# Optimization experiments

Hardware: AMD Instinct MI355X
Metric: run time of the kernel (lower is better)

Reference implementation:

```python
import jax, jax.numpy as jnp
import numpy as np

N, D_IN, D_OUT, E = 100000, 64, 64, 1600000


def setup_inputs() -> dict:
    key = jax.random.key(0)
    k1, k2, k3, k4, k5 = jax.random.split(key, 5)
    x = jax.random.normal(k1, (N, D_IN), dtype=jnp.float32)
    edge_index = jax.random.randint(k2, (2, E), 0, N, dtype=jnp.int64)
    # Linear params (PyTorch default: uniform(-1/sqrt(fan_in), 1/sqrt(fan_in)))
    bound = 1.0 / np.sqrt(D_IN)
    W_self = jax.random.uniform(k3, (D_IN, D_OUT), jnp.float32, -bound, bound)
    b_self = jnp.zeros((D_OUT,), jnp.float32)
    W_neigh = jax.random.uniform(k4, (D_IN, D_OUT), jnp.float32, -bound, bound)
    b_neigh = jax.random.uniform(k5, (D_OUT,), jnp.float32, -bound, bound)
    return {"x": x, "edge_index": edge_index, "W_self": W_self,
            "b_self": b_self, "W_neigh": W_neigh, "b_neigh": b_neigh}


def reference(x, edge_index, W_self, b_self, W_neigh, b_neigh):
    src, dst = edge_index[0], edge_index[1]
    # gather messages from source nodes, scatter-add into destinations
    agg = jax.ops.segment_sum(x[src], dst, num_segments=x.shape[0])  # [N, D_IN]
    # in-degree, clamped to >= 1 (matches bincount().clamp_min(1))
    deg = jax.ops.segment_sum(jnp.ones_like(dst, dtype=x.dtype), dst,
                              num_segments=x.shape[0])
    deg = jnp.maximum(deg, 1.0)[:, None]
    agg = agg / deg
    h = x @ W_self + b_self + agg @ W_neigh + b_neigh
    # dropout is identity in eval mode
    return jax.nn.relu(h)
```

## Files before the change

### kernel.cpp

```cpp
#include <hip/hip_runtime.h>


#define D 64
#define P 256
#define CVTB 1024
#define WTB 4
#define NBMAX 512
#define NP 392
#define BN 256
#define SORTCAP 8160
#define KP 136

typedef __attribute__((ext_vector_type(8))) short bf8_t;
typedef __attribute__((ext_vector_type(4))) float f4_t;

__device__ inline unsigned int bf_rn(float f) {
  unsigned int u = __float_as_uint(f);
  return (u + 0x7FFFu + ((u >> 16) & 1u)) >> 16;
}
__device__ inline unsigned int packbf2(float a, float b) {
  return bf_rn(a) | (bf_rn(b) << 16);
}

__global__ __launch_bounds__(256) void pre_k(const int* __restrict__ dst,
                                             int* __restrict__ hist,
                                             int E, int chunk, int nb,
                                             const float* __restrict__ x,
                                             unsigned short* __restrict__ xbf,
                                             int total4,
                                             const float* __restrict__ Ws,
                                             const float* __restrict__ Wn,
                                             const float* __restrict__ bs,
                                             const float* __restrict__ bn,
                                             unsigned short* __restrict__ wtbf,
                                             float* __restrict__ biasf) {
  __shared__ int h[NBMAX];
  int p = blockIdx.x;
  int t = threadIdx.x;
  if (p < P) {
    for (int i = t; i < NBMAX; i += 256) h[i] = 0;
    __syncthreads();
    int s = p * chunk, e = min(E, s + chunk);
    int n4 = (e - s) >> 2;
    const int4* d4 = (const int4*)(dst + s);
    for (int i = t; i < n4; i += 256) {
      int4 v = d4[i];
      atomicAdd(&h[v.x >> 8], 1);
      atomicAdd(&h[v.y >> 8], 1);
      atomicAdd(&h[v.z >> 8], 1);
      atomicAdd(&h[v.w >> 8], 1);
    }
    for (int i = s + (n4 << 2) + t; i < e; i += 256) atomicAdd(&h[dst[i] >> 8], 1);
    __syncthreads();
    for (int i = t; i < NP; i += 256) hist[p * NP + i] = (i < nb) ? h[i] : 0;
  } else if (p < P + CVTB) {
    int i = (p - P) * 256 + t;
    int stride = CVTB * 256;
    for (; i < total4; i += stride) {
      float4 v = ((const float4*)x)[i];
      uint2 r;
      r.x = packbf2(v.x, v.y);
      r.y = packbf2(v.z, v.w);
      ((uint2*)xbf)[i] = r;
    }
  } else {
    int idx = (p - P - CVTB) * 256 + t;
    int j = idx >> 4, kq = idx & 15, k0 = kq * 8;
    float v[8];
#pragma unroll
    for (int u = 0; u < 8; u++) {
      int k = k0 + u;
      v[u] = (k < 64) ? Ws[k * 64 + j] : Wn[(k - 64) * 64 + j];
    }
    uint4 r;
    r.x = packbf2(v[0], v[1]);
    r.y = packbf2(v[2], v[3]);
    r.z = packbf2(v[4], v[5]);
    r.w = packbf2(v[6], v[7]);
    *(uint4*)&wtbf[j * 128 + k0] = r;
    if (idx < 64) biasf[idx] = bs[idx] + bn[idx];
  }
}

__global__ __launch_bounds__(256) void part_k(const int* __restrict__ ei,
                                              const int* __restrict__ hist,
                                              int* __restrict__ bucketBase,
                                              int* __restrict__ pairs,
                                              int E, int chunk, int nb) {
  __shared__ int cur[NBMAX];
  __shared__ int wsum[4];
  int p = blockIdx.x;
  int t = threadIdx.x;
  int b0 = 2 * t, b1 = 2 * t + 1;
  int c0 = 0, c1 = 0, pr0 = 0, pr1 = 0;
  if (b0 < nb) {
    for (int pp = 0; pp < P; pp++) {
      int2 v = *(const int2*)&hist[pp * NP + b0];
      c0 += v.x; c1 += v.y;
      if (pp < p) { pr0 += v.x; pr1 += v.y; }
    }
  }
  int s = c0 + c1;
  int lane = t & 63, w = t >> 6;
  int inc = s;
  for (int o = 1; o < 64; o <<= 1) {
    int u = __shfl_up(inc, o, 64);
    if (lane >= o) inc += u;
  }
  if (lane == 63) wsum[w] = inc;
  __syncthreads();
  int woff = 0;
  for (int i = 0; i < w; i++) woff += wsum[i];
  int e0 = woff + inc - s;
  if (b0 < nb) {
    cur[b0] = e0 + pr0;
    if (b1 < nb) cur[b1] = e0 + c0 + pr1;
  }
  if (p == 0) {
    if (b0 < nb) bucketBase[b0] = e0;
    if (b1 < nb) bucketBase[b1] = e0 + c0;
    if (t == 255) bucketBase[nb] = woff + inc;
  }
  __syncthreads();
  int st = p * chunk, en = min(E, st + chunk);
  if (((E & 3) == 0)) {
    int n4 = (en - st) >> 2;
    const int4* s4 = (const int4*)(ei + st);
    const int4* d4 = (const int4*)(ei + E + st);
    for (int i = t; i < n4; i += 256) {
      int4 sv = s4[i];
      int4 dv = d4[i];
      int pos;
      pos = atomicAdd(&cur[dv.x >> 8], 1);
      pairs[pos] = sv.x | ((dv.x & (BN - 1)) << 20);
      pos = atomicAdd(&cur[dv.y >> 8], 1);
      pairs[pos] = sv.y | ((dv.y & (BN - 1)) << 20);
      pos = atomicAdd(&cur[dv.z >> 8], 1);
      pairs[pos] = sv.z | ((dv.z & (BN - 1)) << 20);
      pos = atomicAdd(&cur[dv.w >> 8], 1);
      pairs[pos] = sv.w | ((dv.w & (BN - 1)) << 20);
    }
    for (int i = st + (n4 << 2) + t; i < en; i += 256) {
      int src = ei[i], dst = ei[E + i];
      int pos = atomicAdd(&cur[dst >> 8], 1);
      pairs[pos] = src | ((dst & (BN - 1)) << 20);
    }
  } else {
    for (int i = st + t; i < en; i += 256) {
      int src = ei[i], dst = ei[E + i];
      int pos = atomicAdd(&cur[dst >> 8], 1);
      pairs[pos] = src | ((dst & (BN - 1)) << 20);
    }
  }
}

__global__ __launch_bounds__(256) void sort_k(int* __restrict__ pairs,
                                              const int* __restrict__ bucketBase,
                                              int2* __restrict__ spans, int N) {
  __shared__ int stage[SORTCAP];
  __shared__ int cnt[BN];
  __shared__ int off[BN];
  __shared__ int wtot[4];
  int b = blockIdx.x;
  int st = bucketBase[b], en = bucketBase[b + 1];
  int len = en - st;
  if (len > SORTCAP) len = SORTCAP;
  int t = threadIdx.x;
  cnt[t] = 0;
  __syncthreads();
  for (int i = t; i < len; i += 256) {
    int pp = pairs[st + i];
    stage[i] = pp;
    atomicAdd(&cnt[pp >> 20], 1);
  }
  __syncthreads();
  int v = cnt[t];
  int lane = t & 63, w = t >> 6;
  int inc = v;
  for (int o = 1; o < 64; o <<= 1) {
    int u = __shfl_up(inc, o, 64);
    if (lane >= o) inc += u;
  }
  if (lane == 63) wtot[w] = inc;
  __syncthreads();
  int woff = 0;
  for (int i = 0; i < w; i++) woff += wtot[i];
  off[t] = woff + inc - v;
  __syncthreads();
  int node = b * BN + t;
  if (node < N) {
    int s0 = st + off[t];
    spans[node] = make_int2(s0, s0 + v);
  }
  __syncthreads();
  for (int i = t; i < len; i += 256) {
    int pp = stage[i];
    int pos = atomicAdd(&off[pp >> 20], 1);
    pairs[st + pos] = (pp & 0xFFFFF) << 7;
  }
}

__global__ __launch_bounds__(256) void k_agg(const unsigned short* __restrict__ xbf,
                                             const int2* __restrict__ spans,
                                             const int* __restrict__ soff,
                                             unsigned short* __restrict__ aggbf,
                                             int N) {
  int gid = blockIdx.x * blockDim.x + threadIdx.x;
  int lane = threadIdx.x & 63;
  int wave = gid >> 6;
  int nwaves = (gridDim.x * blockDim.x) >> 6;
  int g = lane >> 3, fg = lane & 7;
  const char* xb = (const char*)xbf;
  for (int n8 = wave * 8; n8 < N; n8 += nwaves * 8) {
    int n = n8 + g;
    int2 se = (n < N) ? spans[n] : make_int2(0, 0);
    int st = se.x, en = se.y;
    f4_t e0 = {0.f, 0.f, 0.f, 0.f}, o0 = {0.f, 0.f, 0.f, 0.f};
    f4_t e1 = {0.f, 0.f, 0.f, 0.f}, o1 = {0.f, 0.f, 0.f, 0.f};
    int i = st;
    for (; i + 2 <= en; i += 2) {
      int a0 = soff[i];
      int a1 = soff[i + 1];
      uint4 v0 = *(const uint4*)(xb + (size_t)(unsigned)a0 + fg * 16);
      uint4 v1 = *(const uint4*)(xb + (size_t)(unsigned)a1 + fg * 16);
      f4_t pe, po;
      pe.x = __uint_as_float(v0.x << 16); pe.y = __uint_as_float(v0.y << 16);
      pe.z = __uint_as_float(v0.z << 16); pe.w = __uint_as_float(v0.w << 16);
      po.x = __uint_as_float(v0.x & 0xFFFF0000u); po.y = __uint_as_float(v0.y & 0xFFFF0000u);
      po.z = __uint_as_float(v0.z & 0xFFFF0000u); po.w = __uint_as_float(v0.w & 0xFFFF0000u);
      e0 += pe; o0 += po;
      pe.x = __uint_as_float(v1.x << 16); pe.y = __uint_as_float(v1.y << 16);
      pe.z = __uint_as_float(v1.z << 16); pe.w = __uint_as_float(v1.w << 16);
      po.x = __uint_as_float(v1.x & 0xFFFF0000u); po.y = __uint_as_float(v1.y & 0xFFFF0000u);
      po.z = __uint_as_float(v1.z & 0xFFFF0000u); po.w = __uint_as_float(v1.w & 0xFFFF0000u);
      e1 += pe; o1 += po;
    }
    if (i < en) {
      int a0 = soff[i];
      uint4 v = *(const uint4*)(xb + (size_t)(unsigned)a0 + fg * 16);
      f4_t pe, po;
      pe.x = __uint_as_float(v.x << 16); pe.y = __uint_as_float(v.y << 16);
      pe.z = __uint_as_float(v.z << 16); pe.w = __uint_as_float(v.w << 16);
      po.x = __uint_as_float(v.x & 0xFFFF0000u); po.y = __uint_as_float(v.y & 0xFFFF0000u);
      po.z = __uint_as_float(v.z & 0xFFFF0000u); po.w = __uint_as_float(v.w & 0xFFFF0000u);
      e0 += pe; o0 += po;
    }
    e0 += e1; o0 += o1;
    int len = en - st;
    float inv = 1.f / (float)(len > 0 ? len : 1);
    if (n < N) {
      uint4 r;
      r.x = packbf2(e0.x * inv, o0.x * inv);
      r.y = packbf2(e0.y * inv, o0.y * inv);
      r.z = packbf2(e0.z * inv, o0.z * inv);
      r.w = packbf2(e0.w * inv, o0.w * inv);
      *(uint4*)(aggbf + (size_t)n * D + fg * 8) = r;
    }
  }
}

__global__ __launch_bounds__(256) void k_gemm(const unsigned short* __restrict__ xbf,
                                              const unsigned short* __restrict__ aggbf,
                                              const unsigned short* __restrict__ wtbf,
                                              const float* __restrict__ biasf,
                                              float* __restrict__ out, int ntiles) {
  __shared__ unsigned short sWT[64 * KP];
  __shared__ unsigned short sA[4 * 16 * KP];

  int t = threadIdx.x;
#pragma unroll
  for (int i = 0; i < 4; i++) {
    int idx = i * 256 + t;
    int row = idx >> 4, q = idx & 15;
    *(uint4*)&sWT[row * KP + q * 8] = *(const uint4*)&wtbf[row * 128 + q * 8];
  }
  __syncthreads();

  int w = t >> 6, lane = t & 63;
  int row = lane & 15, part = lane >> 4;
  unsigned short* myA = &sA[w * 16 * KP];

  for (int tile = blockIdx.x * 4 + w; tile < ntiles; tile += gridDim.x * 4) {
    int n0 = tile * 16;
    {
      const unsigned short* srcp =
          (part < 2) ? (xbf + (size_t)(n0 + row) * D + (part & 1) * 32)
                     : (aggbf + (size_t)(n0 + row) * D + (part & 1) * 32);
      const uint4* s4 = (const uint4*)srcp;
      uint4* d4 = (uint4*)&myA[row * KP + part * 32];
      d4[0] = s4[0];
      d4[1] = s4[1];
      d4[2] = s4[2];
      d4[3] = s4[3];
    }
    bf8_t af[4];
#pragma unroll
    for (int kt = 0; kt < 4; kt++)
      af[kt] = *(const bf8_t*)&myA[row * KP + kt * 32 + part * 8];
#pragma unroll
    for (int jt = 0; jt < 4; jt++) {
      f4_t acc = {0.f, 0.f, 0.f, 0.f};
#pragma unroll
      for (int kt = 0; kt < 4; kt++) {
        bf8_t bfr = *(const bf8_t*)&sWT[(jt * 16 + row) * KP + kt * 32 + part * 8];
        acc = __builtin_amdgcn_mfma_f32_16x16x32_bf16(af[kt], bfr, acc, 0, 0, 0);
      }
      int col = jt * 16 + row;
      float bias = biasf[col];
#pragma unroll
      for (int r = 0; r < 4; r++) {
        float v = acc[r] + bias;
        v = v > 0.f ? v : 0.f;
        out[(size_t)(n0 + part * 4 + r) * D + col] = v;
      }
    }
  }
}

extern "C" void kernel_launch(void* const* d_in, const int* in_sizes, int n_in,
                              void* d_out, int out_size, void* d_ws, size_t ws_size,
                              hipStream_t stream) {
  const float* x      = (const float*)d_in[0];
  const int*   ei     = (const int*)d_in[1];
  const float* Wself  = (const float*)d_in[2];
  const float* bself  = (const float*)d_in[3];
  const float* Wneigh = (const float*)d_in[4];
  const float* bneigh = (const float*)d_in[5];

  int N = in_sizes[0] / D;
  int E = in_sizes[1] / 2;
  int nb = (N + BN - 1) / BN;
  int chunk = (((E + P - 1) / P) + 3) & ~3;
  int ntiles = (N + 15) / 16;

  unsigned short* xbf   = (unsigned short*)d_ws;
  unsigned short* aggbf = xbf + (size_t)N * D;
  unsigned short* wtbf  = aggbf + (size_t)N * D;
  float* biasf    = (float*)(wtbf + 64 * 128);
  int2* spans     = (int2*)(biasf + 64);
  int* pairs      = (int*)(spans + N);
  int* hist       = pairs + E;
  int* bucketBase = hist + (size_t)P * NP;

  pre_k<<<P + CVTB + WTB, 256, 0, stream>>>(ei + E, hist, E, chunk, nb,
                                            x, xbf, N * D / 4,
                                            Wself, Wneigh, bself, bneigh,
                                            wtbf, biasf);
  part_k<<<P, 256, 0, stream>>>(ei, hist, bucketBase, pairs, E, chunk, nb);
  sort_k<<<nb, 256, 0, stream>>>(pairs, bucketBase, spans, N);
  k_agg<<<3125, 256, 0, stream>>>(xbf, spans, pairs, aggbf, N);
  k_gemm<<<782, 256, 0, stream>>>(xbf, aggbf, wtbf, biasf, (float*)d_out, ntiles);
}
```

Baseline: 172.4 us.

## Fuse aggregation into GEMM and phase-sort neighbors by source range

Merges the separate gather-aggregate kernel and the GEMM kernel into one kernel. Each wave computes the mean of its 16 nodes' neighbors straight into shared memory, so the bf16 aggregate buffer is never written to or read back from global memory. The sort kernel now sub-bins each destination's edges into 7 source-index phases. In the fused kernel every wave walks the phases in order, which is meant to improve L2 locality of the gathered x rows across concurrently running waves. The costs are 7x larger shared histograms in the sort, a data-dependent while loop that no longer unrolls by two, and only 782 blocks doing the gather instead of 3125.

Result: slower. 196.9 us (+14.2%).

```diff
diff --git a/kernel.cpp b/kernel.cpp
--- a/kernel.cpp
+++ b/kernel.cpp
@@ -10,6 +10,8 @@
 #define BN 256
 #define SORTCAP 8160
 #define KP 136
+#define NPH 7
+#define NBIN (BN * NPH)
 
 typedef __attribute__((ext_vector_type(8))) short bf8_t;
 typedef __attribute__((ext_vector_type(4))) float f4_t;
@@ -158,25 +160,34 @@
                                               const int* __restrict__ bucketBase,
                                               int2* __restrict__ spans, int N) {
   __shared__ int stage[SORTCAP];
-  __shared__ int cnt[BN];
-  __shared__ int off[BN];
+  __shared__ int cnt[NBIN];
+  __shared__ int off[NBIN];
   __shared__ int wtot[4];
   int b = blockIdx.x;
   int st = bucketBase[b], en = bucketBase[b + 1];
   int len = en - st;
   if (len > SORTCAP) len = SORTCAP;
   int t = threadIdx.x;
-  cnt[t] = 0;
+#pragma unroll
+  for (int k = 0; k < NPH; k++) cnt[t * NPH + k] = 0;
   __syncthreads();
   for (int i = t; i < len; i += 256) {
     int pp = pairs[st + i];
     stage[i] = pp;
-    atomicAdd(&cnt[pp >> 20], 1);
-  }
-  __syncthreads();
-  int v = cnt[t];
+    int bin = ((pp >> 20) & 255) * NPH + ((pp >> 14) & 7);
+    atomicAdd(&cnt[bin], 1);
+  }
+  __syncthreads();
+  int base = t * NPH;
+  int c[NPH];
+  int s = 0;
+#pragma unroll
+  for (int k = 0; k < NPH; k++) {
+    c[k] = cnt[base + k];
+    s += c[k];
+  }
   int lane = t & 63, w = t >> 6;
-  int inc = v;
+  int inc = s;
   for (int o = 1; o < 64; o <<= 1) {
     int u = __shfl_up(inc, o, 64);
     if (lane >= o) inc += u;
@@ -185,85 +196,34 @@
   __syncthreads();
   int woff = 0;
   for (int i = 0; i < w; i++) woff += wtot[i];
-  off[t] = woff + inc - v;
-  __syncthreads();
+  int run = woff + inc - s;
+  int nstart = run;
+#pragma unroll
+  for (int k = 0; k < NPH; k++) {
+    off[base + k] = run;
+    run += c[k];
+  }
   int node = b * BN + t;
   if (node < N) {
-    int s0 = st + off[t];
-    spans[node] = make_int2(s0, s0 + v);
+    int s0 = st + nstart;
+    spans[node] = make_int2(s0, s0 + s);
   }
   __syncthreads();
   for (int i = t; i < len; i += 256) {
     int pp = stage[i];
-    int pos = atomicAdd(&off[pp >> 20], 1);
-    pairs[st + pos] = (pp & 0xFFFFF) << 7;
-  }
-}
-
-__global__ __launch_bounds__(256) void k_agg(const unsigned short* __restrict__ xbf,
-                                             const int2* __restrict__ spans,
-                                             const int* __restrict__ soff,
-                                             unsigned short* __restrict__ aggbf,
-                                             int N) {
-  int gid = blockIdx.x * blockDim.x + threadIdx.x;
-  int lane = threadIdx.x & 63;
-  int wave = gid >> 6;
-  int nwaves = (gridDim.x * blockDim.x) >> 6;
-  int g = lane >> 3, fg = lane & 7;
-  const char* xb = (const char*)xbf;
-  for (int n8 = wave * 8; n8 < N; n8 += nwaves * 8) {
-    int n = n8 + g;
-    int2 se = (n < N) ? spans[n] : make_int2(0, 0);
-    int st = se.x, en = se.y;
-    f4_t e0 = {0.f, 0.f, 0.f, 0.f}, o0 = {0.f, 0.f, 0.f, 0.f};
-    f4_t e1 = {0.f, 0.f, 0.f, 0.f}, o1 = {0.f, 0.f, 0.f, 0.f};
-    int i = st;
-    for (; i + 2 <= en; i += 2) {
-      int a0 = soff[i];
-      int a1 = soff[i + 1];
-      uint4 v0 = *(const uint4*)(xb + (size_t)(unsigned)a0 + fg * 16);
-      uint4 v1 = *(const uint4*)(xb + (size_t)(unsigned)a1 + fg * 16);
-      f4_t pe, po;
-      pe.x = __uint_as_float(v0.x << 16); pe.y = __uint_as_float(v0.y << 16);
-      pe.z = __uint_as_float(v0.z << 16); pe.w = __uint_as_float(v0.w << 16);
-      po.x = __uint_as_float(v0.x & 0xFFFF0000u); po.y = __uint_as_float(v0.y & 0xFFFF0000u);
-      po.z = __uint_as_float(v0.z & 0xFFFF0000u); po.w = __uint_as_float(v0.w & 0xFFFF0000u);
-      e0 += pe; o0 += po;
-      pe.x = __uint_as_float(v1.x << 16); pe.y = __uint_as_float(v1.y << 16);
-      pe.z = __uint_as_float(v1.z << 16); pe.w = __uint_as_float(v1.w << 16);
-      po.x = __uint_as_float(v1.x & 0xFFFF0000u); po.y = __uint_as_float(v1.y & 0xFFFF0000u);
-      po.z = __uint_as_float(v1.z & 0xFFFF0000u); po.w = __uint_as_float(v1.w & 0xFFFF0000u);
-      e1 += pe; o1 += po;
-    }
-    if (i < en) {
-      int a0 = soff[i];
-      uint4 v = *(const uint4*)(xb + (size_t)(unsigned)a0 + fg * 16);
-      f4_t pe, po;
-      pe.x = __uint_as_float(v.x << 16); pe.y = __uint_as_float(v.y << 16);
-      pe.z = __uint_as_float(v.z << 16); pe.w = __uint_as_float(v.w << 16);
-      po.x = __uint_as_float(v.x & 0xFFFF0000u); po.y = __uint_as_float(v.y & 0xFFFF0000u);
-      po.z = __uint_as_float(v.z & 0xFFFF0000u); po.w = __uint_as_float(v.w & 0xFFFF0000u);
-      e0 += pe; o0 += po;
-    }
-    e0 += e1; o0 += o1;
-    int len = en - st;
-    float inv = 1.f / (float)(len > 0 ? len : 1);
-    if (n < N) {
-      uint4 r;
-      r.x = packbf2(e0.x * inv, o0.x * inv);
-      r.y = packbf2(e0.y * inv, o0.y * inv);
-      r.z = packbf2(e0.z * inv, o0.z * inv);
-      r.w = packbf2(e0.w * inv, o0.w * inv);
-      *(uint4*)(aggbf + (size_t)n * D + fg * 8) = r;
-    }
-  }
-}
-
-__global__ __launch_bounds__(256) void k_gemm(const unsigned short* __restrict__ xbf,
-                                              const unsigned short* __restrict__ aggbf,
-                                              const unsigned short* __restrict__ wtbf,
-                                              const float* __restrict__ biasf,
-                                              float* __restrict__ out, int ntiles) {
+    int bin = ((pp >> 20) & 255) * NPH + ((pp >> 14) & 7);
+    int pos = atomicAdd(&off[bin], 1);
+    pairs[st + pos] = (pp & 0x1FFFF) << 7;
+  }
+}
+
+__global__ __launch_bounds__(256) void k_aggemm(const unsigned short* __restrict__ xbf,
+                                                const int2* __restrict__ spans,
+                                                const int* __restrict__ soff,
+                                                const unsigned short* __restrict__ wtbf,
+                                                const float* __restrict__ biasf,
+                                                float* __restrict__ out,
+                                                int N, int ntiles) {
   __shared__ unsigned short sWT[64 * KP];
   __shared__ unsigned short sA[4 * 16 * KP];
 
@@ -277,21 +237,55 @@
   __syncthreads();
 
   int w = t >> 6, lane = t & 63;
+  int g = lane >> 3, fg = lane & 7;
   int row = lane & 15, part = lane >> 4;
   unsigned short* myA = &sA[w * 16 * KP];
+  const char* xb = (const char*)xbf;
 
   for (int tile = blockIdx.x * 4 + w; tile < ntiles; tile += gridDim.x * 4) {
     int n0 = tile * 16;
-    {
-      const unsigned short* srcp =
-          (part < 2) ? (xbf + (size_t)(n0 + row) * D + (part & 1) * 32)
-                     : (aggbf + (size_t)(n0 + row) * D + (part & 1) * 32);
-      const uint4* s4 = (const uint4*)srcp;
-      uint4* d4 = (uint4*)&myA[row * KP + part * 32];
-      d4[0] = s4[0];
-      d4[1] = s4[1];
-      d4[2] = s4[2];
-      d4[3] = s4[3];
+#pragma unroll
+    for (int u = 0; u < 2; u++) {
+      int idx = u * 64 + lane;
+      int r = idx >> 3, q = idx & 7;
+      *(uint4*)&myA[r * KP + q * 8] =
+          *(const uint4*)&xbf[(size_t)(n0 + r) * D + q * 8];
+    }
+#pragma unroll
+    for (int sweep = 0; sweep < 2; sweep++) {
+      int n = n0 + sweep * 8 + g;
+      int2 se = (n < N) ? spans[n] : make_int2(0, 0);
+      int st = se.x, en = se.y;
+      f4_t e0 = {0.f, 0.f, 0.f, 0.f}, o0 = {0.f, 0.f, 0.f, 0.f};
+      int i = st;
+      int a0 = (i < en) ? soff[i] : 0x7FFFFFFF;
+      for (int p = 0; p < NPH; p++) {
+        int thr = (p + 1) << 21;
+        while (a0 < thr) {
+          uint4 v = *(const uint4*)(xb + (size_t)(unsigned)a0 + fg * 16);
+          ++i;
+          a0 = (i < en) ? soff[i] : 0x7FFFFFFF;
+          f4_t pe, po;
+          pe.x = __uint_as_float(v.x << 16);
+          pe.y = __uint_as_float(v.y << 16);
+          pe.z = __uint_as_float(v.z << 16);
+          pe.w = __uint_as_float(v.w << 16);
+          po.x = __uint_as_float(v.x & 0xFFFF0000u);
+          po.y = __uint_as_float(v.y & 0xFFFF0000u);
+          po.z = __uint_as_float(v.z & 0xFFFF0000u);
+          po.w = __uint_as_float(v.w & 0xFFFF0000u);
+          e0 += pe;
+          o0 += po;
+        }
+      }
+      int lenn = en - st;
+      float inv = 1.f / (float)(lenn > 0 ? lenn : 1);
+      uint4 rr;
+      rr.x = packbf2(e0.x * inv, o0.x * inv);
+      rr.y = packbf2(e0.y * inv, o0.y * inv);
+      rr.z = packbf2(e0.z * inv, o0.z * inv);
+      rr.w = packbf2(e0.w * inv, o0.w * inv);
+      *(uint4*)&myA[(sweep * 8 + g) * KP + 64 + fg * 8] = rr;
     }
     bf8_t af[4];
 #pragma unroll
@@ -334,8 +328,7 @@
   int ntiles = (N + 15) / 16;
 
   unsigned short* xbf   = (unsigned short*)d_ws;
-  unsigned short* aggbf = xbf + (size_t)N * D;
-  unsigned short* wtbf  = aggbf + (size_t)N * D;
+  unsigned short* wtbf  = xbf + (size_t)N * D;
   float* biasf    = (float*)(wtbf + 64 * 128);
   int2* spans     = (int2*)(biasf + 64);
   int* pairs      = (int*)(spans + N);
@@ -348,6 +341,6 @@
                                             wtbf, biasf);
   part_k<<<P, 256, 0, stream>>>(ei, hist, bucketBase, pairs, E, chunk, nb);
   sort_k<<<nb, 256, 0, stream>>>(pairs, bucketBase, spans, N);
-  k_agg<<<3125, 256, 0, stream>>>(xbf, spans, pairs, aggbf, N);
-  k_gemm<<<782, 256, 0, stream>>>(xbf, aggbf, wtbf, biasf, (float*)d_out, ntiles);
-}
+  k_aggemm<<<782, 256, 0, stream>>>(xbf, spans, pairs, wtbf, biasf,
+                                    (float*)d_out, N, ntiles);
+}
```
